# Performance work log

Measured on AMD Instinct MI355X. Metric: run time of the kernel, lower is better.

The kernel has to match this reference:

```python
import jax, jax.numpy as jnp
import numpy as np

N_WIRES = 14
N_LAYERS = 3
DIM = 2 ** N_WIRES
BATCH = 1024


def _rx(theta):
    # RX(t) = [[cos t/2, -i sin t/2], [-i sin t/2, cos t/2]]
    c = jnp.cos(theta / 2).astype(jnp.complex64)
    s = jnp.sin(theta / 2).astype(jnp.complex64)
    return jnp.stack([jnp.stack([c, -1j * s]), jnp.stack([-1j * s, c])])


def _ry(theta):
    # RY(t) = [[cos t/2, -sin t/2], [sin t/2, cos t/2]]
    c = jnp.cos(theta / 2).astype(jnp.complex64)
    s = jnp.sin(theta / 2).astype(jnp.complex64)
    return jnp.stack([jnp.stack([c, -s]), jnp.stack([s, c])])


def _apply_1q(psi, U, w):
    # psi: (B, 2, 2, ..., 2); apply 2x2 U on qubit axis w+1
    psi = jnp.tensordot(psi, U, axes=((w + 1,), (1,)))  # contracted axis moves to end
    return jnp.moveaxis(psi, -1, w + 1)


def _apply_cnot(psi, c, t):
    # control qubit c, target qubit t (Python ints)
    a0 = jax.lax.index_in_dim(psi, 0, axis=c + 1, keepdims=True)
    a1 = jax.lax.index_in_dim(psi, 1, axis=c + 1, keepdims=True)
    a1 = jnp.flip(a1, axis=t + 1)  # X on target within control=1 subspace
    return jnp.concatenate([a0, a1], axis=c + 1)


def _circuit_features(state, params):
    # state: (B, 2**n) real normalized amplitudes -> PauliZ expvals (B, n)
    n = N_WIRES
    psi = state.astype(jnp.complex64).reshape((-1,) + (2,) * n)
    for layer in range(N_LAYERS):
        for w in range(n):
            psi = _apply_1q(psi, _rx(params[layer, w, 0]), w)
            psi = _apply_1q(psi, _ry(params[layer, w, 1]), w)
        for w in range(n - 1):
            psi = _apply_cnot(psi, w, w + 1)
        psi = _apply_cnot(psi, n - 1, 0)
    probs = jnp.real(psi * jnp.conj(psi))  # (B, 2, ..., 2)
    feats = []
    for w in range(n):
        axes = tuple(a for a in range(1, n + 1) if a != w + 1)
        p = jnp.sum(probs, axis=axes)  # (B, 2)
        feats.append(p[:, 0] - p[:, 1])  # <Z_w>
    return jnp.stack(feats, axis=1)  # (B, n)


def setup_inputs() -> dict:
    key = jax.random.key(0)
    k1, k2, k3 = jax.random.split(key, 3)
    state = jax.random.normal(k1, (BATCH, DIM), dtype=jnp.float32)
    state = state / jnp.linalg.norm(state, axis=1, keepdims=True)  # valid statevectors
    params = jax.random.normal(k2, (N_LAYERS, N_WIRES, 2), dtype=jnp.float32)
    head_w = jax.random.normal(k3, (1, N_WIRES), dtype=jnp.float32) * (1.0 / np.sqrt(N_WIRES))
    head_b = jnp.zeros((1,), dtype=jnp.float32)
    return {"state": state, "params": params, "head_w": head_w, "head_b": head_b}


def reference(state, params, head_w, head_b):
    feats = _circuit_features(state, params)          # (B, n_wires)
    out = feats @ head_w.T + head_b                   # (B, 1)
    return out[:, 0]                                  # (B,)
```

## Files before the change

### kernel.cpp

```cpp
#include <hip/hip_runtime.h>
#include <utility>

#define NW 14
#define NL 3
#define DIM 16384
#define NGATES (NL * NW)
#define TPB 1024
#define NPH (NL * 4)

typedef float v2f __attribute__((ext_vector_type(2)));

struct Phase {
    unsigned short sx[16]  = {};
    unsigned char  pos[12] = {};
    unsigned short vm[4]   = {};
    unsigned char  cpar[4] = {};
    unsigned char  gbase   = 0;
    unsigned char  K       = 0;
};
struct Sched {
    Phase          ph[NPH] = {};
    unsigned short zm[NW]  = {};
};

__host__ __device__ constexpr unsigned foldf(unsigned i) {
    unsigned u = i >> 4;
    return ((u ^ (u >> 2) ^ (u >> 4)) & 1u)
         | (((u ^ (u >> 1) ^ (u >> 3) ^ (u >> 5)) & 1u) << 1)
         | (u & 12u);
}
__host__ __device__ constexpr unsigned sigma(unsigned i) { return i ^ foldf(i); }

constexpr Sched build_sched() {
    Sched sc{};
    unsigned A[NW] = {};
    for (int w = 0; w < NW; ++w) A[w] = 1u << (NW - 1 - w);
    int pidx = 0;
    for (int l = 0; l < NL; ++l) {
        unsigned rows[NW] = {};
        for (int u = 0; u < NW; ++u) rows[u] = A[u] | (1u << (NW + u));
        for (int col = 0; col < NW; ++col) {
            int piv = col;
            while (piv < NW && !((rows[piv] >> col) & 1u)) ++piv;
            if (piv >= NW) continue;
            unsigned tmp = rows[col]; rows[col] = rows[piv]; rows[piv] = tmp;
            for (int r = 0; r < NW; ++r)
                if (r != col && ((rows[r] >> col) & 1u)) rows[r] ^= rows[col];
        }
        unsigned m[NW] = {};
        for (int w = 0; w < NW; ++w) {
            unsigned mk = 0;
            for (int r = 0; r < NW; ++r) mk |= ((rows[r] >> (NW + w)) & 1u) << r;
            m[w] = mk;
        }
        for (int g0 = 0; g0 < NW; g0 += 4) {
            int K = (NW - g0 >= 4) ? 4 : (NW - g0);
            Phase& P = sc.ph[pidx++];
            unsigned mm[4] = { 0, 0, 0, 0 };
            for (int q = 0; q < K; ++q) mm[q] = m[g0 + q];
            for (int s = 0; s < (1 << K); ++s) {
                unsigned v = 0;
                for (int q = 0; q < K; ++q) if ((s >> q) & 1) v ^= mm[q];
                P.sx[s] = (unsigned short)v;
            }
            unsigned pivmask = 0, redv[4] = {}; int pivpos[4] = {};
            for (int q = 0; q < K; ++q) {
                unsigned r = mm[q];
                for (int j = 0; j < q; ++j)
                    if ((r >> pivpos[j]) & 1u) r ^= redv[j];
                int hb = 31 - __builtin_clz(r);
                pivpos[q] = hb; redv[q] = r; pivmask |= 1u << hb;
            }
            int n = 0;
            for (int b = 0; b < NW; ++b)
                if (!((pivmask >> b) & 1u)) P.pos[n++] = (unsigned char)b;
            for (int q = 0; q < K; ++q) {
                P.vm[q] = (unsigned short)A[g0 + q];
                unsigned lowm = (1u << q) - 1u, cp = 0;
                for (int p = 0; p < (1 << K) / 2; ++p) {
                    unsigned s0 = ((p & ~lowm) << 1) | (p & lowm);
                    if (__builtin_popcount(P.sx[s0] & A[g0 + q]) & 1) cp |= 1u << p;
                }
                P.cpar[q] = (unsigned char)cp;
            }
            P.gbase = (unsigned char)(l * NW + g0);
            P.K = (unsigned char)K;
        }
        for (int w = 0; w < NW - 1; ++w) A[w + 1] ^= A[w];
        A[0] ^= A[NW - 1];
    }
    for (int w = 0; w < NW; ++w) sc.zm[w] = (unsigned short)A[w];
    return sc;
}
constexpr Sched SC = build_sched();

template<class F, unsigned... I>
__device__ __forceinline__ void static_for_impl(F&& f, std::integer_sequence<unsigned, I...>) {
    (f(std::integral_constant<unsigned, I>{}), ...);
}
template<unsigned N, class F>
__device__ __forceinline__ void static_for(F&& f) {
    static_for_impl(static_cast<F&&>(f), std::make_integer_sequence<unsigned, N>{});
}

template<int NEGLO, int NEGHI>
__device__ __forceinline__ v2f cmul(v2f k, v2f x) {
    v2f y;
    if constexpr (!NEGLO)
        asm("v_pk_mul_f32 %0, %1, %2 op_sel:[0,0] op_sel_hi:[0,1]"
            : "=&v"(y) : "v"(k), "v"(x));
    else
        asm("v_pk_mul_f32 %0, %1, %2 op_sel:[0,0] op_sel_hi:[0,1] neg_lo:[1,0] neg_hi:[1,0]"
            : "=&v"(y) : "v"(k), "v"(x));
    if constexpr (!NEGHI)
        asm("v_pk_fma_f32 %0, %1, %2, %0 op_sel:[1,1,0] op_sel_hi:[1,0,1] neg_lo:[0,1,0]"
            : "+v"(y) : "v"(k), "v"(x));
    else
        asm("v_pk_fma_f32 %0, %1, %2, %0 op_sel:[1,1,0] op_sel_hi:[1,0,1] neg_lo:[1,1,0] neg_hi:[1,0,0]"
            : "+v"(y) : "v"(k), "v"(x));
    return y;
}
template<int NEGLO, int NEGHI>
__device__ __forceinline__ void cmac(v2f& y, v2f k, v2f x) {
    if constexpr (!NEGLO)
        asm("v_pk_fma_f32 %0, %1, %2, %0 op_sel:[0,0,0] op_sel_hi:[0,1,1]"
            : "+v"(y) : "v"(k), "v"(x));
    else
        asm("v_pk_fma_f32 %0, %1, %2, %0 op_sel:[0,0,0] op_sel_hi:[0,1,1] neg_lo:[1,0,0] neg_hi:[1,0,0]"
            : "+v"(y) : "v"(k), "v"(x));
    if constexpr (!NEGHI)
        asm("v_pk_fma_f32 %0, %1, %2, %0 op_sel:[1,1,0] op_sel_hi:[1,0,1] neg_lo:[0,1,0]"
            : "+v"(y) : "v"(k), "v"(x));
    else
        asm("v_pk_fma_f32 %0, %1, %2, %0 op_sel:[1,1,0] op_sel_hi:[1,0,1] neg_lo:[1,1,0] neg_hi:[1,0,0]"
            : "+v"(y) : "v"(k), "v"(x));
}

template<int PIDX>
__device__ __forceinline__ void apply_phase(char* psiB, const float4* __restrict__ umat,
                                            unsigned tid)
{
    constexpr int K    = SC.ph[PIDX].K;
    constexpr int NLOC = 1 << K;
    constexpr int NIT  = DIM / (NLOC * TPB);
    __syncthreads();
#pragma unroll
    for (int it = 0; it < NIT; ++it) {
        const unsigned idx = tid + it * TPB;
        unsigned rep = 0;
#pragma unroll
        for (int b = 0; b < 14 - K; ++b)
            rep |= ((idx >> b) & 1u) << SC.ph[PIDX].pos[b];
        const unsigned srep8 = (rep ^ foldf(rep)) << 3;

        v2f x[NLOC];
        static_for<NLOC>([&](auto S) {
            constexpr unsigned s   = decltype(S)::value;
            constexpr unsigned off = sigma(SC.ph[PIDX].sx[s]) << 3;
            x[s] = *(const v2f*)(psiB + (srep8 ^ off));
        });

        static_for<K>([&](auto Qc) {
            constexpr unsigned q  = decltype(Qc)::value;
            constexpr unsigned vm = SC.ph[PIDX].vm[q];
            constexpr unsigned cp = SC.ph[PIDX].cpar[q];
            const float4 u = umat[SC.ph[PIDX].gbase + q];
            const unsigned sm = ((unsigned)__popc(rep & vm)) << 31;
            v2f A, B;
            A.x = u.x; A.y = __uint_as_float(__float_as_uint(u.y) ^ sm);
            B.x = __uint_as_float(__float_as_uint(u.z) ^ sm); B.y = u.w;
            static_for<NLOC / 2>([&](auto Pc) {
                constexpr unsigned p    = decltype(Pc)::value;
                constexpr unsigned lowm = (1u << q) - 1u;
                constexpr unsigned s0   = ((p & ~lowm) << 1) | (p & lowm);
                constexpr unsigned s1   = s0 | (1u << q);
                constexpr bool     c    = (cp >> p) & 1u;
                const v2f x0 = x[s0], x1 = x[s1];
                if constexpr (!c) {
                    v2f y0 = cmul<0, 0>(A, x0); cmac<0, 0>(y0, B, x1);
                    v2f y1 = cmul<1, 0>(B, x0); cmac<0, 1>(y1, A, x1);
                    x[s0] = y0; x[s1] = y1;
                } else {
                    v2f y0 = cmul<0, 1>(A, x0); cmac<1, 0>(y0, B, x1);
                    v2f y1 = cmul<0, 0>(B, x0); cmac<0, 0>(y1, A, x1);
                    x[s0] = y0; x[s1] = y1;
                }
            });
        });

        static_for<NLOC>([&](auto S) {
            constexpr unsigned s   = decltype(S)::value;
            constexpr unsigned off = sigma(SC.ph[PIDX].sx[s]) << 3;
            *(v2f*)(psiB + (srep8 ^ off)) = x[s];
        });
    }
}

__global__ __launch_bounds__(TPB) void qsim_kernel(
    const float* __restrict__ state,
    const float* __restrict__ params,
    const float* __restrict__ head_w,
    const float* __restrict__ head_b,
    float* __restrict__ out)
{
    __shared__ v2f    psi[DIM];
    __shared__ float4 umat[NGATES];
    __shared__ float  red[TPB / 64];
    char* psiB = (char*)psi;

    const unsigned tid = threadIdx.x;

    if (tid < NGATES) {
        float t1 = 0.5f * params[2 * tid + 0];
        float t2 = 0.5f * params[2 * tid + 1];
        float s1, c1, s2, c2;
        sincosf(t1, &s1, &c1);
        sincosf(t2, &s2, &c2);
        umat[tid] = make_float4(c1 * c2, s1 * s2, -s2 * c1, -c2 * s1);
    }

    const float4* st4 = reinterpret_cast<const float4*>(state) + (size_t)blockIdx.x * (DIM / 4);
#pragma unroll
    for (int k = 0; k < DIM / 4 / TPB; ++k) {
        unsigned idx = tid + k * TPB;
        float4 v = st4[idx];
        unsigned a = idx * 4;
        unsigned b = (a ^ foldf(a)) << 3;
        *(v2f*)(psiB + (b ^ 0))  = (v2f){ v.x, 0.f };
        *(v2f*)(psiB + (b ^ 8))  = (v2f){ v.y, 0.f };
        *(v2f*)(psiB + (b ^ 16)) = (v2f){ v.z, 0.f };
        *(v2f*)(psiB + (b ^ 24)) = (v2f){ v.w, 0.f };
    }

    static_for<NPH>([&](auto Pi) {
        apply_phase<(int)decltype(Pi)::value>(psiB, umat, tid);
    });

    __syncthreads();

    const unsigned baseB = (tid ^ foldf(tid)) << 3;
    float hws[NW];
#pragma unroll
    for (int w = 0; w < NW; ++w) {
        float hw = head_w[w];
        hws[w] = (__popc(tid & (SC.zm[w] & (TPB - 1))) & 1) ? -hw : hw;
    }
    float acc = 0.f;
#pragma unroll
    for (int k = 0; k < DIM / TPB; ++k) {
        float c = 0.f;
#pragma unroll
        for (int w = 0; w < NW; ++w)
            c += (__popc((unsigned)k & (SC.zm[w] >> 10)) & 1) ? -hws[w] : hws[w];
        v2f a = *(const v2f*)(psiB + baseB + k * (TPB * 8));
        acc += (a.x * a.x + a.y * a.y) * c;
    }

#pragma unroll
    for (int off = 32; off > 0; off >>= 1)
        acc += __shfl_down(acc, off, 64);
    const unsigned lane = tid & 63, wv = tid >> 6;
    if (lane == 0) red[wv] = acc;
    __syncthreads();
    if (tid == 0) {
        float tot = 0.f;
#pragma unroll
        for (int i = 0; i < TPB / 64; ++i) tot += red[i];
        out[blockIdx.x] = tot + head_b[0];
    }
}

extern "C" void kernel_launch(void* const* d_in, const int* in_sizes, int n_in,
                              void* d_out, int out_size, void* d_ws, size_t ws_size,
                              hipStream_t stream) {
    const float* state  = (const float*)d_in[0];
    const float* params = (const float*)d_in[1];
    const float* head_w = (const float*)d_in[2];
    const float* head_b = (const float*)d_in[3];
    float* out = (float*)d_out;

    qsim_kernel<<<out_size, TPB, 0, stream>>>(state, params, head_w, head_b, out);
}
```

Baseline: 139.3 us.

## Fuse state load into first gate phase and batch coset iterations per thread

The first phase now reads the real input amplitudes straight from global memory into registers and applies its first gate with real-only packed multiplies. This drops the separate LDS initialization pass and one read-write round trip. All phases now process every coset of a thread together in one unrolled block, so loads, gate math and stores overlap better, at the cost of more registers. The readout computes the per-k sign-weighted head coefficients with a small Walsh-Hadamard butterfly instead of a per-k popcount loop.

```diff
diff --git a/kernel.cpp b/kernel.cpp
--- a/kernel.cpp
+++ b/kernel.cpp
@@ -135,65 +135,133 @@
         asm("v_pk_fma_f32 %0, %1, %2, %0 op_sel:[1,1,0] op_sel_hi:[1,0,1] neg_lo:[1,1,0] neg_hi:[1,0,0]"
             : "+v"(y) : "v"(k), "v"(x));
 }
-
-template<int PIDX>
+template<int NEGLO, int NEGHI>
+__device__ __forceinline__ v2f rmul(v2f k, v2f rr) {
+    v2f y;
+    if constexpr (!NEGLO && !NEGHI)
+        asm("v_pk_mul_f32 %0, %1, %2"
+            : "=v"(y) : "v"(k), "v"(rr));
+    else if constexpr (NEGLO && !NEGHI)
+        asm("v_pk_mul_f32 %0, %1, %2 neg_lo:[1,0]"
+            : "=v"(y) : "v"(k), "v"(rr));
+    else if constexpr (!NEGLO && NEGHI)
+        asm("v_pk_mul_f32 %0, %1, %2 neg_hi:[1,0]"
+            : "=v"(y) : "v"(k), "v"(rr));
+    else
+        asm("v_pk_mul_f32 %0, %1, %2 neg_lo:[1,0] neg_hi:[1,0]"
+            : "=v"(y) : "v"(k), "v"(rr));
+    return y;
+}
+template<int NEGLO, int NEGHI>
+__device__ __forceinline__ void rmac(v2f& y, v2f k, v2f rr) {
+    if constexpr (!NEGLO && !NEGHI)
+        asm("v_pk_fma_f32 %0, %1, %2, %0"
+            : "+v"(y) : "v"(k), "v"(rr));
+    else if constexpr (NEGLO && !NEGHI)
+        asm("v_pk_fma_f32 %0, %1, %2, %0 neg_lo:[1,0,0]"
+            : "+v"(y) : "v"(k), "v"(rr));
+    else if constexpr (!NEGLO && NEGHI)
+        asm("v_pk_fma_f32 %0, %1, %2, %0 neg_hi:[1,0,0]"
+            : "+v"(y) : "v"(k), "v"(rr));
+    else
+        asm("v_pk_fma_f32 %0, %1, %2, %0 neg_lo:[1,0,0] neg_hi:[1,0,0]"
+            : "+v"(y) : "v"(k), "v"(rr));
+}
+
+template<int PIDX, bool FIRST>
 __device__ __forceinline__ void apply_phase(char* psiB, const float4* __restrict__ umat,
-                                            unsigned tid)
+                                            unsigned tid, const float* __restrict__ gsrc)
 {
     constexpr int K    = SC.ph[PIDX].K;
     constexpr int NLOC = 1 << K;
-    constexpr int NIT  = DIM / (NLOC * TPB);
+    constexpr int NCOS = 16 / NLOC;
     __syncthreads();
-#pragma unroll
-    for (int it = 0; it < NIT; ++it) {
-        const unsigned idx = tid + it * TPB;
+
+    unsigned repv[NCOS], sb[NCOS];
+    static_for<NCOS>([&](auto Cc) {
+        constexpr unsigned c = decltype(Cc)::value;
+        const unsigned idx = tid + c * TPB;
         unsigned rep = 0;
 #pragma unroll
         for (int b = 0; b < 14 - K; ++b)
             rep |= ((idx >> b) & 1u) << SC.ph[PIDX].pos[b];
-        const unsigned srep8 = (rep ^ foldf(rep)) << 3;
-
-        v2f x[NLOC];
-        static_for<NLOC>([&](auto S) {
-            constexpr unsigned s   = decltype(S)::value;
-            constexpr unsigned off = sigma(SC.ph[PIDX].sx[s]) << 3;
-            x[s] = *(const v2f*)(psiB + (srep8 ^ off));
-        });
-
-        static_for<K>([&](auto Qc) {
-            constexpr unsigned q  = decltype(Qc)::value;
-            constexpr unsigned vm = SC.ph[PIDX].vm[q];
-            constexpr unsigned cp = SC.ph[PIDX].cpar[q];
-            const float4 u = umat[SC.ph[PIDX].gbase + q];
-            const unsigned sm = ((unsigned)__popc(rep & vm)) << 31;
+        repv[c] = rep;
+        sb[c] = (rep ^ foldf(rep)) << 3;
+    });
+
+    v2f x[16];
+    v2f rr[16];
+    if constexpr (FIRST) {
+        static_for<16>([&](auto Sc) {
+            constexpr unsigned s = decltype(Sc)::value;
+            constexpr unsigned m = SC.ph[PIDX].sx[s];
+            float v = gsrc[repv[0] ^ m];
+            rr[s] = (v2f){ v, v };
+        });
+    } else {
+        static_for<NCOS>([&](auto Cc) {
+            constexpr unsigned c = decltype(Cc)::value;
+            static_for<NLOC>([&](auto Sc) {
+                constexpr unsigned s   = decltype(Sc)::value;
+                constexpr unsigned off = sigma(SC.ph[PIDX].sx[s]) << 3;
+                x[c * NLOC + s] = *(const v2f*)(psiB + (sb[c] ^ off));
+            });
+        });
+    }
+
+    static_for<K>([&](auto Qc) {
+        constexpr unsigned q  = decltype(Qc)::value;
+        constexpr unsigned vm = SC.ph[PIDX].vm[q];
+        constexpr unsigned cp = SC.ph[PIDX].cpar[q];
+        const float4 u = umat[SC.ph[PIDX].gbase + q];
+        static_for<NCOS>([&](auto Cc) {
+            constexpr unsigned c = decltype(Cc)::value;
+            const unsigned sm = ((unsigned)__popc(repv[c] & vm)) << 31;
             v2f A, B;
             A.x = u.x; A.y = __uint_as_float(__float_as_uint(u.y) ^ sm);
             B.x = __uint_as_float(__float_as_uint(u.z) ^ sm); B.y = u.w;
             static_for<NLOC / 2>([&](auto Pc) {
                 constexpr unsigned p    = decltype(Pc)::value;
                 constexpr unsigned lowm = (1u << q) - 1u;
-                constexpr unsigned s0   = ((p & ~lowm) << 1) | (p & lowm);
+                constexpr unsigned b0   = ((p & ~lowm) << 1) | (p & lowm);
+                constexpr unsigned s0   = b0 + c * NLOC;
                 constexpr unsigned s1   = s0 | (1u << q);
-                constexpr bool     c    = (cp >> p) & 1u;
-                const v2f x0 = x[s0], x1 = x[s1];
-                if constexpr (!c) {
-                    v2f y0 = cmul<0, 0>(A, x0); cmac<0, 0>(y0, B, x1);
-                    v2f y1 = cmul<1, 0>(B, x0); cmac<0, 1>(y1, A, x1);
-                    x[s0] = y0; x[s1] = y1;
+                constexpr bool     rc   = (cp >> p) & 1u;
+                if constexpr (FIRST && q == 0) {
+                    const v2f r0 = rr[s0], r1 = rr[s1];
+                    if constexpr (!rc) {
+                        v2f y0 = rmul<0, 0>(A, r0); rmac<0, 0>(y0, B, r1);
+                        v2f y1 = rmul<1, 0>(B, r0); rmac<0, 1>(y1, A, r1);
+                        x[s0] = y0; x[s1] = y1;
+                    } else {
+                        v2f y0 = rmul<0, 1>(A, r0); rmac<1, 0>(y0, B, r1);
+                        v2f y1 = rmul<0, 0>(B, r0); rmac<0, 0>(y1, A, r1);
+                        x[s0] = y0; x[s1] = y1;
+                    }
                 } else {
-                    v2f y0 = cmul<0, 1>(A, x0); cmac<1, 0>(y0, B, x1);
-                    v2f y1 = cmul<0, 0>(B, x0); cmac<0, 0>(y1, A, x1);
-                    x[s0] = y0; x[s1] = y1;
+                    const v2f x0 = x[s0], x1 = x[s1];
+                    if constexpr (!rc) {
+                        v2f y0 = cmul<0, 0>(A, x0); cmac<0, 0>(y0, B, x1);
+                        v2f y1 = cmul<1, 0>(B, x0); cmac<0, 1>(y1, A, x1);
+                        x[s0] = y0; x[s1] = y1;
+                    } else {
+                        v2f y0 = cmul<0, 1>(A, x0); cmac<1, 0>(y0, B, x1);
+                        v2f y1 = cmul<0, 0>(B, x0); cmac<0, 0>(y1, A, x1);
+                        x[s0] = y0; x[s1] = y1;
+                    }
                 }
             });
         });
-
-        static_for<NLOC>([&](auto S) {
-            constexpr unsigned s   = decltype(S)::value;
+    });
+
+    static_for<NCOS>([&](auto Cc) {
+        constexpr unsigned c = decltype(Cc)::value;
+        static_for<NLOC>([&](auto Sc) {
+            constexpr unsigned s   = decltype(Sc)::value;
             constexpr unsigned off = sigma(SC.ph[PIDX].sx[s]) << 3;
-            *(v2f*)(psiB + (srep8 ^ off)) = x[s];
-        });
-    }
+            *(v2f*)(psiB + (sb[c] ^ off)) = x[c * NLOC + s];
+        });
+    });
 }
 
 __global__ __launch_bounds__(TPB) void qsim_kernel(
@@ -219,42 +287,46 @@
         umat[tid] = make_float4(c1 * c2, s1 * s2, -s2 * c1, -c2 * s1);
     }
 
-    const float4* st4 = reinterpret_cast<const float4*>(state) + (size_t)blockIdx.x * (DIM / 4);
-#pragma unroll
-    for (int k = 0; k < DIM / 4 / TPB; ++k) {
-        unsigned idx = tid + k * TPB;
-        float4 v = st4[idx];
-        unsigned a = idx * 4;
-        unsigned b = (a ^ foldf(a)) << 3;
-        *(v2f*)(psiB + (b ^ 0))  = (v2f){ v.x, 0.f };
-        *(v2f*)(psiB + (b ^ 8))  = (v2f){ v.y, 0.f };
-        *(v2f*)(psiB + (b ^ 16)) = (v2f){ v.z, 0.f };
-        *(v2f*)(psiB + (b ^ 24)) = (v2f){ v.w, 0.f };
-    }
-
-    static_for<NPH>([&](auto Pi) {
-        apply_phase<(int)decltype(Pi)::value>(psiB, umat, tid);
+    const float* gsrc = state + (size_t)blockIdx.x * DIM;
+    apply_phase<0, true>(psiB, umat, tid, gsrc);
+    static_for<NPH - 1>([&](auto Pi) {
+        apply_phase<(int)decltype(Pi)::value + 1, false>(psiB, umat, tid, gsrc);
     });
 
     __syncthreads();
 
+    float e[NW];
+    static_for<NW>([&](auto Wc) {
+        constexpr int      w    = decltype(Wc)::value;
+        constexpr unsigned zlow = SC.zm[w] & (TPB - 1);
+        float hw = head_w[w];
+        e[w] = (__popc(tid & zlow) & 1) ? -hw : hw;
+    });
+    float c[16];
+    static_for<16>([&](auto Mc) { c[decltype(Mc)::value] = 0.f; });
+    static_for<NW>([&](auto Wc) {
+        constexpr int      w = decltype(Wc)::value;
+        constexpr unsigned m = SC.zm[w] >> 10;
+        c[m] += e[w];
+    });
+    static_for<4>([&](auto Bc) {
+        constexpr unsigned B = 1u << decltype(Bc)::value;
+        static_for<16>([&](auto Kc) {
+            constexpr unsigned k = decltype(Kc)::value;
+            if constexpr (!(k & B)) {
+                float a = c[k], b = c[k | B];
+                c[k] = a + b; c[k | B] = a - b;
+            }
+        });
+    });
+
     const unsigned baseB = (tid ^ foldf(tid)) << 3;
-    float hws[NW];
-#pragma unroll
-    for (int w = 0; w < NW; ++w) {
-        float hw = head_w[w];
-        hws[w] = (__popc(tid & (SC.zm[w] & (TPB - 1))) & 1) ? -hw : hw;
-    }
     float acc = 0.f;
-#pragma unroll
-    for (int k = 0; k < DIM / TPB; ++k) {
-        float c = 0.f;
-#pragma unroll
-        for (int w = 0; w < NW; ++w)
-            c += (__popc((unsigned)k & (SC.zm[w] >> 10)) & 1) ? -hws[w] : hws[w];
+    static_for<16>([&](auto Kc) {
+        constexpr int k = decltype(Kc)::value;
         v2f a = *(const v2f*)(psiB + baseB + k * (TPB * 8));
-        acc += (a.x * a.x + a.y * a.y) * c;
-    }
+        acc += (a.x * a.x + a.y * a.y) * c[k];
+    });
 
 #pragma unroll
     for (int off = 32; off > 0; off >>= 1)
```

New measurement: 141.9 us. About the same (+1.9%).

## Fuse gate phases into superphases using DPP lane exchanges and register-resident readout

Applied to the files above, without the earlier changes.

Replaces the 12 per-layer four-gate phases with compile-time superphases of up to 8 gates each. Four gates act on register-held amplitudes and up to four act across neighbouring lanes via DPP swaps, so there are fewer round trips through LDS and fewer barriers. The layout for each superphase is chosen by a compile-time randomized search that aims to avoid bank conflicts on both the read and write sides. The final expectation value is computed directly from registers with a Walsh-Hadamard sign table instead of re-reading LDS. The cost is a much more complex constexpr schedule and higher register pressure from 16 complex values per thread.

```diff
diff --git a/kernel.cpp b/kernel.cpp
--- a/kernel.cpp
+++ b/kernel.cpp
@@ -4,95 +4,210 @@
 #define NW 14
 #define NL 3
 #define DIM 16384
-#define NGATES (NL * NW)
+#define NG  (NL * NW)
 #define TPB 1024
-#define NPH (NL * 4)
+#define MAXSP 12
 
 typedef float v2f __attribute__((ext_vector_type(2)));
 
-struct Phase {
-    unsigned short sx[16]  = {};
-    unsigned char  pos[12] = {};
-    unsigned short vm[4]   = {};
-    unsigned char  cpar[4] = {};
-    unsigned char  gbase   = 0;
-    unsigned char  K       = 0;
+struct SP {
+    int J = 0, nr = 0, nl = 0;
+    unsigned dirs[4]  = {};
+    unsigned traw[10] = {};
+    unsigned tR[10] = {}, tW[10] = {};
+    unsigned sxR[16] = {}, sxW[16] = {};
+    unsigned pv[8]   = {};
+    unsigned cpar[8] = {};
+    unsigned gid[8]  = {};
+    int wflag = 1;
 };
-struct Sched {
-    Phase          ph[NPH] = {};
-    unsigned short zm[NW]  = {};
+struct Sched2 {
+    int nsp = 0;
+    SP sp[MAXSP] = {};
+    unsigned stA[10] = {};
+    unsigned stK[4]  = {};
+    unsigned pz[NW]  = {};
+    unsigned nib[NW] = {};
+    int ok = 1;
 };
 
-__host__ __device__ constexpr unsigned foldf(unsigned i) {
-    unsigned u = i >> 4;
-    return ((u ^ (u >> 2) ^ (u >> 4)) & 1u)
-         | (((u ^ (u >> 1) ^ (u >> 3) ^ (u >> 5)) & 1u) << 1)
-         | (u & 12u);
-}
-__host__ __device__ constexpr unsigned sigma(unsigned i) { return i ^ foldf(i); }
-
-constexpr Sched build_sched() {
-    Sched sc{};
-    unsigned A[NW] = {};
-    for (int w = 0; w < NW; ++w) A[w] = 1u << (NW - 1 - w);
-    int pidx = 0;
-    for (int l = 0; l < NL; ++l) {
-        unsigned rows[NW] = {};
-        for (int u = 0; u < NW; ++u) rows[u] = A[u] | (1u << (NW + u));
-        for (int col = 0; col < NW; ++col) {
-            int piv = col;
-            while (piv < NW && !((rows[piv] >> col) & 1u)) ++piv;
-            if (piv >= NW) continue;
-            unsigned tmp = rows[col]; rows[col] = rows[piv]; rows[piv] = tmp;
-            for (int r = 0; r < NW; ++r)
-                if (r != col && ((rows[r] >> col) & 1u)) rows[r] ^= rows[col];
-        }
-        unsigned m[NW] = {};
-        for (int w = 0; w < NW; ++w) {
-            unsigned mk = 0;
-            for (int r = 0; r < NW; ++r) mk |= ((rows[r] >> (NW + w)) & 1u) << r;
-            m[w] = mk;
-        }
-        for (int g0 = 0; g0 < NW; g0 += 4) {
-            int K = (NW - g0 >= 4) ? 4 : (NW - g0);
-            Phase& P = sc.ph[pidx++];
-            unsigned mm[4] = { 0, 0, 0, 0 };
-            for (int q = 0; q < K; ++q) mm[q] = m[g0 + q];
-            for (int s = 0; s < (1 << K); ++s) {
-                unsigned v = 0;
-                for (int q = 0; q < K; ++q) if ((s >> q) & 1) v ^= mm[q];
-                P.sx[s] = (unsigned short)v;
-            }
-            unsigned pivmask = 0, redv[4] = {}; int pivpos[4] = {};
-            for (int q = 0; q < K; ++q) {
-                unsigned r = mm[q];
-                for (int j = 0; j < q; ++j)
-                    if ((r >> pivpos[j]) & 1u) r ^= redv[j];
-                int hb = 31 - __builtin_clz(r);
-                pivpos[q] = hb; redv[q] = r; pivmask |= 1u << hb;
-            }
-            int n = 0;
-            for (int b = 0; b < NW; ++b)
-                if (!((pivmask >> b) & 1u)) P.pos[n++] = (unsigned char)b;
-            for (int q = 0; q < K; ++q) {
-                P.vm[q] = (unsigned short)A[g0 + q];
-                unsigned lowm = (1u << q) - 1u, cp = 0;
-                for (int p = 0; p < (1 << K) / 2; ++p) {
-                    unsigned s0 = ((p & ~lowm) << 1) | (p & lowm);
-                    if (__builtin_popcount(P.sx[s0] & A[g0 + q]) & 1) cp |= 1u << p;
+constexpr unsigned fap(const unsigned* g, unsigned x) {
+    unsigned r = 0;
+    for (int b = 4; b < 14; ++b) if ((x >> b) & 1u) r ^= g[b - 4];
+    return x ^ r;
+}
+constexpr int rank4n(const unsigned* v) {
+    unsigned bas[4] = {}; int nb = 0;
+    for (int i = 0; i < 4; ++i) {
+        unsigned r = v[i] & 15u;
+        for (int j = 0; j < nb; ++j) {
+            int hb = 3; while (hb > 0 && !((bas[j] >> hb) & 1u)) --hb;
+            if ((r >> hb) & 1u) r ^= bas[j];
+        }
+        if (r) bas[nb++] = r;
+    }
+    return nb;
+}
+
+constexpr Sched2 build2() {
+    Sched2 S{};
+    unsigned mk[NG] = {}, vmg[NG] = {}, zm[NW] = {};
+    {
+        unsigned A[NW] = {};
+        for (int w = 0; w < NW; ++w) A[w] = 1u << (NW - 1 - w);
+        int g = 0;
+        for (int l = 0; l < NL; ++l) {
+            unsigned rows[NW] = {};
+            for (int u = 0; u < NW; ++u) rows[u] = A[u] | (1u << (NW + u));
+            for (int col = 0; col < NW; ++col) {
+                int piv = col;
+                while (piv < NW && !((rows[piv] >> col) & 1u)) ++piv;
+                if (piv >= NW) { S.ok = 0; continue; }
+                unsigned tmp = rows[col]; rows[col] = rows[piv]; rows[piv] = tmp;
+                for (int r = 0; r < NW; ++r)
+                    if (r != col && ((rows[r] >> col) & 1u)) rows[r] ^= rows[col];
+            }
+            for (int w = 0; w < NW; ++w) {
+                unsigned m = 0;
+                for (int r = 0; r < NW; ++r) m |= ((rows[r] >> (NW + w)) & 1u) << r;
+                mk[g] = m; vmg[g] = A[w]; ++g;
+            }
+            for (int w = 0; w < NW - 1; ++w) A[w + 1] ^= A[w];
+            A[0] ^= A[NW - 1];
+        }
+        for (int w = 0; w < NW; ++w) zm[w] = A[w];
+    }
+    int gs = 0;
+    while (gs < NG && S.nsp < MAXSP) {
+        SP& P = S.sp[S.nsp];
+        unsigned bas[14] = {}; int nb = 0;
+        int j = gs;
+        while (j < NG && (j - gs) < 8) {
+            unsigned r = mk[j];
+            for (int i = 0; i < nb; ++i) {
+                int hb = 13; while (hb > 0 && !((bas[i] >> hb) & 1u)) --hb;
+                if ((r >> hb) & 1u) r ^= bas[i];
+            }
+            if (!r) break;
+            bas[nb++] = r; ++j;
+        }
+        P.J = j - gs; P.nr = P.J < 4 ? P.J : 4; P.nl = P.J - P.nr;
+        for (int q = 0; q < P.J; ++q) P.gid[q] = (unsigned)(gs + q);
+        for (int q = 0; q < P.nr; ++q) P.dirs[q] = mk[gs + q];
+        for (int q = P.nr; q < 4; ++q) {
+            for (int b = 0; b < NW; ++b) {
+                unsigned r = 1u << b;
+                for (int i = 0; i < nb; ++i) {
+                    int hb = 13; while (hb > 0 && !((bas[i] >> hb) & 1u)) --hb;
+                    if ((r >> hb) & 1u) r ^= bas[i];
                 }
-                P.cpar[q] = (unsigned char)cp;
-            }
-            P.gbase = (unsigned char)(l * NW + g0);
-            P.K = (unsigned char)K;
-        }
-        for (int w = 0; w < NW - 1; ++w) A[w + 1] ^= A[w];
-        A[0] ^= A[NW - 1];
-    }
-    for (int w = 0; w < NW; ++w) sc.zm[w] = (unsigned short)A[w];
-    return sc;
-}
-constexpr Sched SC = build_sched();
+                if (r) { bas[nb++] = r; P.dirs[q] = 1u << b; break; }
+            }
+        }
+        unsigned lm[4] = {};
+        for (int i = 0; i < P.nl; ++i) lm[i] = mk[gs + 4 + i];
+        unsigned tt[4] = { 0, 0, 0, 0 };
+        if (P.nl > 0) tt[0] = lm[0];
+        if (P.nl > 1) tt[1] = lm[1];
+        if (P.nl > 2) tt[2] = lm[2] ^ tt[0] ^ tt[1];
+        if (P.nl > 3) tt[3] = lm[3] ^ lm[2];
+        for (int i = P.nl; i < 4; ++i) {
+            for (int b = 0; b < NW; ++b) {
+                unsigned r = 1u << b;
+                for (int k2 = 0; k2 < nb; ++k2) {
+                    int hb = 13; while (hb > 0 && !((bas[k2] >> hb) & 1u)) --hb;
+                    if ((r >> hb) & 1u) r ^= bas[k2];
+                }
+                if (r) { bas[nb++] = r; tt[i] = 1u << b; break; }
+            }
+        }
+        for (int i = 0; i < 4; ++i) P.traw[i] = tt[i];
+        for (int b6 = 4; b6 < 10; ++b6) {
+            for (int b = 0; b < NW; ++b) {
+                unsigned r = 1u << b;
+                for (int k2 = 0; k2 < nb; ++k2) {
+                    int hb = 13; while (hb > 0 && !((bas[k2] >> hb) & 1u)) --hb;
+                    if ((r >> hb) & 1u) r ^= bas[k2];
+                }
+                if (r) { bas[nb++] = r; P.traw[b6] = 1u << b; break; }
+            }
+        }
+        if (nb != 14) S.ok = 0;
+        for (int q = 0; q < P.J; ++q) {
+            unsigned vm = vmg[gs + q], p = 0;
+            for (int b = 0; b < 10; ++b)
+                if (__builtin_popcount(P.traw[b] & vm) & 1) p |= 1u << b;
+            P.pv[q] = p;
+            unsigned cp = 0;
+            for (int s = 0; s < 16; ++s) {
+                unsigned sx = 0;
+                for (int q2 = 0; q2 < 4; ++q2) if ((s >> q2) & 1) sx ^= P.dirs[q2];
+                if (__builtin_popcount(sx & vm) & 1) cp |= 1u << s;
+            }
+            P.cpar[q] = cp;
+        }
+        ++S.nsp; gs = j;
+    }
+    if (gs < NG) S.ok = 0;
+    S.sp[S.nsp - 1].wflag = 0;
+    for (int t = 0; t < S.nsp; ++t) {
+        unsigned wd[4] = {}, rd[4] = {};
+        if (t == 0) { wd[0] = 4; wd[1] = 8; wd[2] = 16; wd[3] = 32; }
+        else for (int i = 0; i < 4; ++i) wd[i] = S.sp[t - 1].traw[i];
+        for (int i = 0; i < 4; ++i) rd[i] = S.sp[t].traw[i];
+        unsigned bg[10] = {}; int bscore = -1;
+        for (unsigned seed = 0; seed < 512u; ++seed) {
+            unsigned g[10] = {};
+            if (seed) {
+                for (int b = 0; b < 10; ++b) {
+                    unsigned h = (seed * 2654435761u) ^ ((unsigned)(b + 3) * 0x9E3779B9u);
+                    h ^= h >> 16; h *= 2246822519u; h ^= h >> 13;
+                    g[b] = h & 15u;
+                }
+            }
+            unsigned W[4] = {}, R[4] = {};
+            for (int i = 0; i < 4; ++i) { W[i] = fap(g, wd[i]); R[i] = fap(g, rd[i]); }
+            int sc = rank4n(W) + rank4n(R);
+            if (sc > bscore) {
+                bscore = sc;
+                for (int b = 0; b < 10; ++b) bg[b] = g[b];
+                if (sc == 8) break;
+            }
+        }
+        for (int b = 0; b < 10; ++b) S.sp[t].tR[b] = fap(bg, S.sp[t].traw[b]);
+        for (int s = 0; s < 16; ++s) {
+            unsigned sx = 0;
+            for (int q = 0; q < 4; ++q) if ((s >> q) & 1) sx ^= S.sp[t].dirs[q];
+            S.sp[t].sxR[s] = fap(bg, sx);
+        }
+        if (t == 0) {
+            for (int b = 0; b < 10; ++b) S.stA[b] = fap(bg, 4u << b);
+            for (int k = 0; k < 4; ++k) S.stK[k] = fap(bg, (unsigned)k << 12);
+        } else {
+            for (int b = 0; b < 10; ++b) S.sp[t - 1].tW[b] = fap(bg, S.sp[t - 1].traw[b]);
+            for (int s = 0; s < 16; ++s) {
+                unsigned sx = 0;
+                for (int q = 0; q < 4; ++q) if ((s >> q) & 1) sx ^= S.sp[t - 1].dirs[q];
+                S.sp[t - 1].sxW[s] = fap(bg, sx);
+            }
+        }
+    }
+    for (int w = 0; w < NW; ++w) {
+        const SP& L = S.sp[S.nsp - 1];
+        unsigned p = 0;
+        for (int b = 0; b < 10; ++b)
+            if (__builtin_popcount(L.traw[b] & zm[w]) & 1) p |= 1u << b;
+        S.pz[w] = p;
+        unsigned nv = 0;
+        for (int q = 0; q < 4; ++q)
+            if (__builtin_popcount(L.dirs[q] & zm[w]) & 1) nv |= 1u << q;
+        S.nib[w] = nv;
+    }
+    return S;
+}
+constexpr Sched2 SC2 = build2();
+static_assert(SC2.ok == 1, "schedule build failed");
+static_assert(SC2.nsp <= MAXSP, "too many superphases");
 
 template<class F, unsigned... I>
 __device__ __forceinline__ void static_for_impl(F&& f, std::integer_sequence<unsigned, I...>) {
@@ -135,64 +250,84 @@
         asm("v_pk_fma_f32 %0, %1, %2, %0 op_sel:[1,1,0] op_sel_hi:[1,0,1] neg_lo:[1,1,0] neg_hi:[1,0,0]"
             : "+v"(y) : "v"(k), "v"(x));
 }
+template<bool CS> __device__ __forceinline__ v2f  cmulA(v2f k, v2f x) { return cmul<0, CS ? 1 : 0>(k, x); }
+template<bool CS> __device__ __forceinline__ void cmacB(v2f& y, v2f k, v2f x) { cmac<CS ? 1 : 0, 0>(y, k, x); }
+
+constexpr int lane_ctrl(int li) {
+    return li == 0 ? 0xB1 : li == 1 ? 0x4E : li == 2 ? 0x141 : 0x140;
+}
+template<int CTRL>
+__device__ __forceinline__ v2f dppx(v2f x) {
+    int lo = __builtin_amdgcn_update_dpp(0, __float_as_int(x.x), CTRL, 0xf, 0xf, false);
+    int hi = __builtin_amdgcn_update_dpp(0, __float_as_int(x.y), CTRL, 0xf, 0xf, false);
+    return (v2f){ __int_as_float(lo), __int_as_float(hi) };
+}
 
 template<int PIDX>
-__device__ __forceinline__ void apply_phase(char* psiB, const float4* __restrict__ umat,
-                                            unsigned tid)
+__device__ __forceinline__ void apply_sp(char* psiB, const float4* __restrict__ umat,
+                                         unsigned tid, v2f* x)
 {
-    constexpr int K    = SC.ph[PIDX].K;
-    constexpr int NLOC = 1 << K;
-    constexpr int NIT  = DIM / (NLOC * TPB);
-    __syncthreads();
-#pragma unroll
-    for (int it = 0; it < NIT; ++it) {
-        const unsigned idx = tid + it * TPB;
-        unsigned rep = 0;
-#pragma unroll
-        for (int b = 0; b < 14 - K; ++b)
-            rep |= ((idx >> b) & 1u) << SC.ph[PIDX].pos[b];
-        const unsigned srep8 = (rep ^ foldf(rep)) << 3;
-
-        v2f x[NLOC];
-        static_for<NLOC>([&](auto S) {
-            constexpr unsigned s   = decltype(S)::value;
-            constexpr unsigned off = sigma(SC.ph[PIDX].sx[s]) << 3;
-            x[s] = *(const v2f*)(psiB + (srep8 ^ off));
-        });
-
-        static_for<K>([&](auto Qc) {
-            constexpr unsigned q  = decltype(Qc)::value;
-            constexpr unsigned vm = SC.ph[PIDX].vm[q];
-            constexpr unsigned cp = SC.ph[PIDX].cpar[q];
-            const float4 u = umat[SC.ph[PIDX].gbase + q];
-            const unsigned sm = ((unsigned)__popc(rep & vm)) << 31;
+    unsigned frep = 0;
+    static_for<10>([&](auto Bc) {
+        constexpr int b = (int)decltype(Bc)::value;
+        constexpr unsigned mm = SC2.sp[PIDX].tR[b] |
+                                (SC2.sp[PIDX].wflag ? (SC2.sp[PIDX].tW[b] << 16) : 0u);
+        frep ^= mm & (unsigned)(-(int)((tid >> b) & 1u));
+    });
+    const unsigned srepR8 = (frep & 0x3FFFu) << 3;
+    const unsigned srepW8 = ((frep >> 16) & 0x3FFFu) << 3;
+
+    static_for<16>([&](auto Sc) {
+        constexpr unsigned s = decltype(Sc)::value;
+        constexpr unsigned off = SC2.sp[PIDX].sxR[s] << 3;
+        x[s] = *(const v2f*)(psiB + (srepR8 ^ off));
+    });
+    if constexpr (SC2.sp[PIDX].wflag)
+        __syncthreads();
+
+    static_for<8>([&](auto Qc) {
+        constexpr int q = (int)decltype(Qc)::value;
+        if constexpr (q < SC2.sp[PIDX].J) {
+            constexpr unsigned cp = SC2.sp[PIDX].cpar[q];
+            constexpr unsigned pv = SC2.sp[PIDX].pv[q];
+            const float4 u = umat[SC2.sp[PIDX].gid[q]];
+            const unsigned sm = ((unsigned)__popc(tid & pv)) << 31;
             v2f A, B;
             A.x = u.x; A.y = __uint_as_float(__float_as_uint(u.y) ^ sm);
             B.x = __uint_as_float(__float_as_uint(u.z) ^ sm); B.y = u.w;
-            static_for<NLOC / 2>([&](auto Pc) {
-                constexpr unsigned p    = decltype(Pc)::value;
-                constexpr unsigned lowm = (1u << q) - 1u;
-                constexpr unsigned s0   = ((p & ~lowm) << 1) | (p & lowm);
-                constexpr unsigned s1   = s0 | (1u << q);
-                constexpr bool     c    = (cp >> p) & 1u;
-                const v2f x0 = x[s0], x1 = x[s1];
-                if constexpr (!c) {
-                    v2f y0 = cmul<0, 0>(A, x0); cmac<0, 0>(y0, B, x1);
-                    v2f y1 = cmul<1, 0>(B, x0); cmac<0, 1>(y1, A, x1);
+            if constexpr (q < SC2.sp[PIDX].nr) {
+                static_for<8>([&](auto Pc) {
+                    constexpr unsigned p    = decltype(Pc)::value;
+                    constexpr unsigned lowm = (1u << q) - 1u;
+                    constexpr unsigned s0   = ((p & ~lowm) << 1) | (p & lowm);
+                    constexpr unsigned s1   = s0 | (1u << q);
+                    constexpr bool c0 = (cp >> s0) & 1u;
+                    constexpr bool c1 = (cp >> s1) & 1u;
+                    const v2f x0 = x[s0], x1 = x[s1];
+                    v2f y0 = cmulA<c0>(A, x0); cmacB<c0>(y0, B, x1);
+                    v2f y1 = cmulA<c1>(A, x1); cmacB<c1>(y1, B, x0);
                     x[s0] = y0; x[s1] = y1;
-                } else {
-                    v2f y0 = cmul<0, 1>(A, x0); cmac<1, 0>(y0, B, x1);
-                    v2f y1 = cmul<0, 0>(B, x0); cmac<0, 0>(y1, A, x1);
-                    x[s0] = y0; x[s1] = y1;
-                }
-            });
+                });
+            } else {
+                constexpr int ctrl = lane_ctrl(q - SC2.sp[PIDX].nr);
+                static_for<16>([&](auto Sc) {
+                    constexpr unsigned s = decltype(Sc)::value;
+                    constexpr bool cs = (cp >> s) & 1u;
+                    v2f recv = dppx<ctrl>(x[s]);
+                    v2f y = cmulA<cs>(A, x[s]); cmacB<cs>(y, B, recv);
+                    x[s] = y;
+                });
+            }
+        }
+    });
+
+    if constexpr (SC2.sp[PIDX].wflag) {
+        static_for<16>([&](auto Sc) {
+            constexpr unsigned s = decltype(Sc)::value;
+            constexpr unsigned off = SC2.sp[PIDX].sxW[s] << 3;
+            *(v2f*)(psiB + (srepW8 ^ off)) = x[s];
         });
-
-        static_for<NLOC>([&](auto S) {
-            constexpr unsigned s   = decltype(S)::value;
-            constexpr unsigned off = sigma(SC.ph[PIDX].sx[s]) << 3;
-            *(v2f*)(psiB + (srep8 ^ off)) = x[s];
-        });
+        __syncthreads();
     }
 }
 
@@ -204,13 +339,12 @@
     float* __restrict__ out)
 {
     __shared__ v2f    psi[DIM];
-    __shared__ float4 umat[NGATES];
+    __shared__ float4 umat[NG];
     __shared__ float  red[TPB / 64];
     char* psiB = (char*)psi;
-
     const unsigned tid = threadIdx.x;
 
-    if (tid < NGATES) {
+    if (tid < NG) {
         float t1 = 0.5f * params[2 * tid + 0];
         float t2 = 0.5f * params[2 * tid + 1];
         float s1, c1, s2, c2;
@@ -219,42 +353,58 @@
         umat[tid] = make_float4(c1 * c2, s1 * s2, -s2 * c1, -c2 * s1);
     }
 
+    unsigned tpart = 0;
+    static_for<10>([&](auto Bc) {
+        constexpr int b = (int)decltype(Bc)::value;
+        constexpr unsigned m = SC2.stA[b];
+        tpart ^= m & (unsigned)(-(int)((tid >> b) & 1u));
+    });
     const float4* st4 = reinterpret_cast<const float4*>(state) + (size_t)blockIdx.x * (DIM / 4);
-#pragma unroll
-    for (int k = 0; k < DIM / 4 / TPB; ++k) {
-        unsigned idx = tid + k * TPB;
-        float4 v = st4[idx];
-        unsigned a = idx * 4;
-        unsigned b = (a ^ foldf(a)) << 3;
-        *(v2f*)(psiB + (b ^ 0))  = (v2f){ v.x, 0.f };
-        *(v2f*)(psiB + (b ^ 8))  = (v2f){ v.y, 0.f };
-        *(v2f*)(psiB + (b ^ 16)) = (v2f){ v.z, 0.f };
-        *(v2f*)(psiB + (b ^ 24)) = (v2f){ v.w, 0.f };
-    }
-
-    static_for<NPH>([&](auto Pi) {
-        apply_phase<(int)decltype(Pi)::value>(psiB, umat, tid);
-    });
-
+    static_for<4>([&](auto Kc) {
+        constexpr int k = (int)decltype(Kc)::value;
+        float4 v = st4[tid + k * TPB];
+        const unsigned bb = (tpart ^ SC2.stK[k]) << 3;
+        *(v2f*)(psiB + (bb ^ (0u << 3))) = (v2f){ v.x, 0.f };
+        *(v2f*)(psiB + (bb ^ (1u << 3))) = (v2f){ v.y, 0.f };
+        *(v2f*)(psiB + (bb ^ (2u << 3))) = (v2f){ v.z, 0.f };
+        *(v2f*)(psiB + (bb ^ (3u << 3))) = (v2f){ v.w, 0.f };
+    });
     __syncthreads();
 
-    const unsigned baseB = (tid ^ foldf(tid)) << 3;
-    float hws[NW];
-#pragma unroll
-    for (int w = 0; w < NW; ++w) {
+    v2f x[16];
+    static_for<MAXSP>([&](auto Pc) {
+        constexpr int p = (int)decltype(Pc)::value;
+        if constexpr (p < SC2.nsp) apply_sp<p>(psiB, umat, tid, x);
+    });
+
+    float e[NW];
+    static_for<NW>([&](auto Wc) {
+        constexpr int w = (int)decltype(Wc)::value;
+        constexpr unsigned pzw = SC2.pz[w];
         float hw = head_w[w];
-        hws[w] = (__popc(tid & (SC.zm[w] & (TPB - 1))) & 1) ? -hw : hw;
-    }
+        e[w] = (__popc(tid & pzw) & 1) ? -hw : hw;
+    });
+    float c[16];
+    static_for<16>([&](auto Mc) { c[decltype(Mc)::value] = 0.f; });
+    static_for<NW>([&](auto Wc) {
+        constexpr int w = (int)decltype(Wc)::value;
+        c[SC2.nib[w]] += e[w];
+    });
+    static_for<4>([&](auto Bc) {
+        constexpr unsigned B = 1u << decltype(Bc)::value;
+        static_for<16>([&](auto Kc) {
+            constexpr unsigned k = decltype(Kc)::value;
+            if constexpr (!(k & B)) {
+                float a = c[k], b = c[k | B];
+                c[k] = a + b; c[k | B] = a - b;
+            }
+        });
+    });
     float acc = 0.f;
-#pragma unroll
-    for (int k = 0; k < DIM / TPB; ++k) {
-        float c = 0.f;
-#pragma unroll
-        for (int w = 0; w < NW; ++w)
-            c += (__popc((unsigned)k & (SC.zm[w] >> 10)) & 1) ? -hws[w] : hws[w];
-        v2f a = *(const v2f*)(psiB + baseB + k * (TPB * 8));
-        acc += (a.x * a.x + a.y * a.y) * c;
-    }
+    static_for<16>([&](auto Sc) {
+        constexpr int s = (int)decltype(Sc)::value;
+        acc += (x[s].x * x[s].x + x[s].y * x[s].y) * c[s];
+    });
 
 #pragma unroll
     for (int off = 32; off > 0; off >>= 1)
```

Result: slower. 157.9 us (+13.3%).
